# Kernel optimization log

Measured on AMD Instinct MI355X. Metric: run time of the kernel, lower is better.

The kernel has to match this reference:

```python
import jax, jax.numpy as jnp
import numpy as np

MARGIN = 0.1
NEG_INF = -1e30


def _l2norm(x):
    return x / jnp.linalg.norm(x, axis=1, keepdims=True)


def setup_inputs() -> dict:
    key = jax.random.key(0)
    ks = jax.random.split(key, 6)
    d, nNeg, Q = 128, 10, 32
    triplet_len = nNeg + 2
    n = Q * triplet_len            # 384
    m = 65536                      # XBM memory bank size
    V = 2048                       # image-id space
    P, Nn = 10, 25                 # pos / hard-neg list lengths per query
    inputs_col = _l2norm(jax.random.normal(ks[0], (n, d), dtype=jnp.float32))
    inputs_row = _l2norm(jax.random.normal(ks[1], (m, d), dtype=jnp.float32))
    targets_row = jax.random.randint(ks[2], (m,), 0, V, dtype=jnp.int64)
    qidxs = jnp.arange(Q, dtype=jnp.int64) + V  # unique query ids, disjoint from db ids
    targets_col = jax.random.randint(ks[3], (n,), 0, V, dtype=jnp.int64)
    targets_col = targets_col.at[jnp.arange(0, n, triplet_len)].set(qidxs)
    pidxs = jax.random.randint(ks[4], (Q, P), 0, V, dtype=jnp.int64)
    nnegs = jax.random.randint(ks[5], (Q, Nn), 0, V, dtype=jnp.int64)
    return {"inputs_col": inputs_col, "inputs_row": inputs_row,
            "targets_col": targets_col, "targets_row": targets_row,
            "qidxs": qidxs, "pidxs": pidxs, "nnegs": nnegs, "nNeg": nNeg}


def reference(inputs_col, inputs_row, targets_col, targets_row, qidxs, pidxs, nnegs, nNeg):
    n = inputs_col.shape[0]
    triplet_len = nNeg + 2
    query_list = jnp.arange(0, n, triplet_len)          # [Q]
    Q = query_list.shape[0]
    query_idx = targets_col[query_list]                 # [Q]

    sim_mat = inputs_col @ inputs_row.T                 # [n, m]
    sims = sim_mat[query_list]                          # [Q, m]

    # per-query lookup of pos / neg id lists (qidxs are unique)
    qidx_local = jnp.argmax(qidxs[None, :] == query_idx[:, None], axis=1)
    this_pidx = pidxs[qidx_local]                       # [Q, P]
    this_nneg = nnegs[qidx_local]                       # [Q, Nn]

    # from_batch handling (only possible when shapes match; here memory-bank case)
    if targets_col.shape[0] == targets_row.shape[0]:
        fb = jnp.all(targets_col == targets_row)
        trc = jnp.where(fb, targets_row.at[query_list].set(-1), targets_row)
    else:
        fb = None
        trc = targets_row

    # isin masks, vectorized across queries: [Q, m]
    pos_mask = jnp.any(targets_row[None, :, None] == this_pidx[:, None, :], axis=-1)
    neg_mask = ~jnp.any(trc[None, :, None] == this_nneg[:, None, :], axis=-1)
    if fb is not None:
        neg_mask = jnp.where(fb, neg_mask.at[:, query_list].set(False), neg_mask)

    # sort was only used to read the max -> masked max suffices
    pos_max = jnp.max(jnp.where(pos_mask, sims, NEG_INF), axis=1)   # [Q]
    neg_max = jnp.max(jnp.where(neg_mask, sims, NEG_INF), axis=1)   # [Q]

    pos_sel = pos_mask & (sims < neg_max[:, None] + MARGIN)
    neg_sel = neg_mask & (sims > jnp.maximum(0.4, pos_max)[:, None] - MARGIN)

    pos_cnt = jnp.sum(pos_sel, axis=1)
    neg_cnt = jnp.sum(neg_sel, axis=1)
    pos_loss = jnp.where(pos_cnt > 0,
                         jnp.sum(jnp.where(pos_sel, 1.0 - sims, 0.0), axis=1) / jnp.maximum(pos_cnt, 1),
                         0.0)
    neg_loss = jnp.where(neg_cnt > 0,
                         jnp.sum(jnp.where(neg_sel, sims, 0.0), axis=1) / jnp.maximum(neg_cnt, 1),
                         0.0)

    has_pos = jnp.any(pos_mask, axis=1)                 # whole block skipped if no positives
    loss = jnp.sum(jnp.where(has_pos, pos_loss + neg_loss, 0.0)) / Q
    return loss
```

## Files before the change

### kernel.cpp

```cpp
#include <hip/hip_runtime.h>

#define NEG_INF_F (-1e30f)
#define MARGIN_F 0.1f
#define TABN 4096
#define BR 256
#define NT 512

__device__ __forceinline__ unsigned fkey(float f) {
    unsigned b = __float_as_uint(f);
    return (b & 0x80000000u) ? ~b : (b | 0x80000000u);
}
__device__ __forceinline__ float fdec(unsigned k) {
    unsigned b = (k & 0x80000000u) ? (k ^ 0x80000000u) : ~k;
    return __uint_as_float(b);
}

__global__ __launch_bounds__(256) void setup_kernel(
    const float* __restrict__ inputs_col,
    const int* __restrict__ targets_col,
    const int* __restrict__ qidxs,
    const int* __restrict__ pidxs,
    const int* __restrict__ nnegs,
    unsigned* __restrict__ ptab,
    unsigned* __restrict__ ntab,
    float* __restrict__ qT,
    float* __restrict__ accums,
    unsigned* __restrict__ bar,
    int d, int Q, int P, int Nn, int triplet_len)
{
    __shared__ int qmap[32];
    const int tid = threadIdx.x;

    if (tid < Q) {
        int t = targets_col[tid * triplet_len];
        int l = 0;
        for (int i = Q - 1; i >= 0; --i) if (qidxs[i] == t) l = i;
        qmap[tid] = l;
    }
    for (int i = tid; i < TABN; i += 256) { ptab[i] = 0u; ntab[i] = 0u; }
    if (tid < 160) accums[tid] = 0.f;
    if (tid < 2) bar[tid] = 0u;
    __syncthreads();

    for (int i = tid; i < Q * P; i += 256) {
        int q = i / P, k = i - q * P;
        int id = pidxs[qmap[q] * P + k];
        if ((unsigned)id < TABN) atomicOr(&ptab[id], 1u << q);
    }
    for (int i = tid; i < Q * Nn; i += 256) {
        int q = i / Nn, k = i - q * Nn;
        int id = nnegs[qmap[q] * Nn + k];
        if ((unsigned)id < TABN) atomicOr(&ntab[id], 1u << q);
    }
    for (int i = tid; i < d * Q; i += 256) {
        int dd = i >> 5, q = i & 31;
        qT[i] = inputs_col[(size_t)(q * triplet_len) * d + dd];
    }
}

__device__ __forceinline__ void gsync(unsigned* cnt, unsigned nblk) {
    __syncthreads();
    if (threadIdx.x == 0) {
        __threadfence();
        atomicAdd(cnt, 1u);
        while (__hip_atomic_load(cnt, __ATOMIC_RELAXED, __HIP_MEMORY_SCOPE_AGENT) < nblk)
            __builtin_amdgcn_s_sleep(2);
        __threadfence();
    }
    __syncthreads();
}

__global__ __launch_bounds__(NT, 2) void fused_kernel(
    const float* __restrict__ qT,
    const float* __restrict__ rows,
    const int* __restrict__ targets_row,
    const unsigned* __restrict__ ptab,
    const unsigned* __restrict__ ntab,
    float* __restrict__ gmax,
    float* __restrict__ accums,
    unsigned* __restrict__ bar,
    float* __restrict__ out,
    int m, int nb)
{
    __shared__ float qv[128][32];
    __shared__ float rt[32][261];
    __shared__ unsigned pbm[BR], nbm[BR];
    __shared__ unsigned spk[32], snk[32];
    __shared__ float thr[2][32];
    __shared__ float wpart[8][32][5];
    __shared__ int islast;

    const int tid = threadIdx.x;
    const int bid = blockIdx.x;
    const int j0 = bid * BR;

    for (int i = tid; i < 128 * 32; i += NT) qv[i >> 5][i & 31] = qT[i];
    if (tid < 32) { spk[tid] = fkey(NEG_INF_F); snk[tid] = fkey(NEG_INF_F); }
    if (tid < BR) {
        int j = j0 + tid;
        unsigned pb = 0u, nbv = 0u;
        if (j < m) {
            int t = targets_row[j];
            if ((unsigned)t < TABN) { pb = ptab[t]; nbv = ~ntab[t]; }
            else                    { nbv = ~0u; }
        }
        pbm[tid] = pb; nbm[tid] = nbv;
    }

    const int qg = tid & 7;
    const int rg = tid >> 3;
    const int kk = tid & 7;
    const int jj = tid >> 3;

    float acc[4][4];
#pragma unroll
    for (int a = 0; a < 4; ++a)
#pragma unroll
        for (int b = 0; b < 4; ++b) acc[a][b] = 0.f;

    for (int kc = 0; kc < 128; kc += 32) {
        __syncthreads();
#pragma unroll
        for (int p = 0; p < 4; ++p) {
            int j = j0 + jj + 64 * p;
            int jc = (j < m) ? j : (m - 1);
            float4 v = *(const float4*)&rows[(size_t)jc * 128 + kc + 4 * kk];
            rt[4 * kk + 0][jj + 64 * p] = v.x;
            rt[4 * kk + 1][jj + 64 * p] = v.y;
            rt[4 * kk + 2][jj + 64 * p] = v.z;
            rt[4 * kk + 3][jj + 64 * p] = v.w;
        }
        __syncthreads();
#pragma unroll
        for (int k = 0; k < 32; ++k) {
            float4 qf = *(const float4*)&qv[kc + k][qg * 4];
            float4 rf = *(const float4*)&rt[k][rg * 4];
            const float* qp = (const float*)&qf;
            const float* rp = (const float*)&rf;
#pragma unroll
            for (int qi = 0; qi < 4; ++qi)
#pragma unroll
                for (int ri = 0; ri < 4; ++ri)
                    acc[qi][ri] = fmaf(qp[qi], rp[ri], acc[qi][ri]);
        }
    }

    unsigned pb[4], nbr[4];
#pragma unroll
    for (int r = 0; r < 4; ++r) { pb[r] = pbm[rg * 4 + r]; nbr[r] = nbm[rg * 4 + r]; }

#pragma unroll
    for (int qi = 0; qi < 4; ++qi) {
        const int q = qg * 4 + qi;
        float pmax = NEG_INF_F, nmax = NEG_INF_F;
#pragma unroll
        for (int r = 0; r < 4; ++r) {
            if ((pb[r] >> q) & 1u)  pmax = fmaxf(pmax, acc[qi][r]);
            if ((nbr[r] >> q) & 1u) nmax = fmaxf(nmax, acc[qi][r]);
        }
#pragma unroll
        for (int off = 32; off >= 8; off >>= 1) {
            pmax = fmaxf(pmax, __shfl_down(pmax, off));
            nmax = fmaxf(nmax, __shfl_down(nmax, off));
        }
        if ((tid & 63) < 8) {
            atomicMax(&spk[q], fkey(pmax));
            atomicMax(&snk[q], fkey(nmax));
        }
    }
    __syncthreads();
    if (tid < 64) {
        int side = tid >> 5, q = tid & 31;
        gmax[(size_t)tid * nb + bid] = fdec(side ? snk[q] : spk[q]);
    }

    gsync(&bar[0], (unsigned)nb);

    {
        int p = tid >> 3, c = tid & 7;
        float mv = NEG_INF_F;
        for (int b = c; b < nb; b += 8) mv = fmaxf(mv, gmax[(size_t)p * nb + b]);
#pragma unroll
        for (int msk = 1; msk <= 4; msk <<= 1) mv = fmaxf(mv, __shfl_xor(mv, msk));
        if (c == 0) thr[p >> 5][p & 31] = mv;
    }
    __syncthreads();

    const int wave = tid >> 6, lane = tid & 63;
#pragma unroll
    for (int qi = 0; qi < 4; ++qi) {
        const int q = qg * 4 + qi;
        const float posThr = thr[1][q] + MARGIN_F;
        const float negThr = fmaxf(0.4f, thr[0][q]) - MARGIN_F;
        float ps = 0.f, pc = 0.f, ns = 0.f, nc = 0.f, pmc = 0.f;
#pragma unroll
        for (int r = 0; r < 4; ++r) {
            float s = acc[qi][r];
            unsigned pm = (pb[r] >> q) & 1u;
            unsigned nm = (nbr[r] >> q) & 1u;
            pmc += (float)pm;
            if (pm && s < posThr) { ps += 1.f - s; pc += 1.f; }
            if (nm && s > negThr) { ns += s;       nc += 1.f; }
        }
#pragma unroll
        for (int off = 32; off >= 8; off >>= 1) {
            ps  += __shfl_down(ps, off);
            pc  += __shfl_down(pc, off);
            ns  += __shfl_down(ns, off);
            nc  += __shfl_down(nc, off);
            pmc += __shfl_down(pmc, off);
        }
        if (lane < 8) {
            wpart[wave][lane * 4 + qi][0] = ps;
            wpart[wave][lane * 4 + qi][1] = pc;
            wpart[wave][lane * 4 + qi][2] = ns;
            wpart[wave][lane * 4 + qi][3] = nc;
            wpart[wave][lane * 4 + qi][4] = pmc;
        }
    }
    __syncthreads();
    if (tid < 160) {
        float v = 0.f;
#pragma unroll
        for (int w = 0; w < 8; ++w) v += wpart[w][tid / 5][tid % 5];
        atomicAdd(&accums[tid], v);
    }

    __syncthreads();
    if (tid == 0) {
        __threadfence();
        unsigned old = atomicAdd(&bar[1], 1u);
        islast = (old == (unsigned)(nb - 1)) ? 1 : 0;
    }
    __syncthreads();
    if (islast) {
        if (tid == 0) __threadfence();
        __syncthreads();
        if (tid < 64) {
            float v = 0.f;
            if (tid < 32) {
                float psv = accums[tid * 5 + 0];
                float pcv = accums[tid * 5 + 1];
                float nsv = accums[tid * 5 + 2];
                float ncv = accums[tid * 5 + 3];
                float pmc = accums[tid * 5 + 4];
                float pl = (pcv > 0.f) ? psv / pcv : 0.f;
                float nl = (ncv > 0.f) ? nsv / ncv : 0.f;
                v = (pmc > 0.f) ? (pl + nl) : 0.f;
            }
#pragma unroll
            for (int off = 32; off; off >>= 1) v += __shfl_down(v, off);
            if (tid == 0) out[0] = v / 32.0f;
        }
    }
}

extern "C" void kernel_launch(void* const* d_in, const int* in_sizes, int n_in,
                              void* d_out, int out_size, void* d_ws, size_t ws_size,
                              hipStream_t stream)
{
    const float* inputs_col = (const float*)d_in[0];
    const float* inputs_row = (const float*)d_in[1];
    const int* targets_col  = (const int*)d_in[2];
    const int* targets_row  = (const int*)d_in[3];
    const int* qidxs        = (const int*)d_in[4];
    const int* pidxs        = (const int*)d_in[5];
    const int* nnegs        = (const int*)d_in[6];

    const int n  = in_sizes[2];
    int m        = in_sizes[3];
    const int Q  = in_sizes[4];
    const int P  = in_sizes[5] / Q;
    const int Nn = in_sizes[6] / Q;
    const int d  = in_sizes[0] / n;
    const int triplet_len = n / Q;

    int nb = (m + BR - 1) / BR;

    char* ws = (char*)d_ws;
    size_t off = 0;
    unsigned* ptab = (unsigned*)(ws + off); off += (size_t)TABN * 4;
    unsigned* ntab = (unsigned*)(ws + off); off += (size_t)TABN * 4;
    float* qT      = (float*)(ws + off);    off += (size_t)d * Q * 4;
    float* gmax    = (float*)(ws + off);    off += (size_t)64 * nb * 4;
    float* accums  = (float*)(ws + off);    off += (size_t)160 * 4;
    unsigned* bar  = (unsigned*)(ws + off); off += 2 * 4;
    float* out     = (float*)d_out;

    setup_kernel<<<1, 256, 0, stream>>>(inputs_col, targets_col, qidxs, pidxs, nnegs,
                                        ptab, ntab, qT, accums, bar,
                                        d, Q, P, Nn, triplet_len);

    fused_kernel<<<nb, NT, 0, stream>>>(qT, inputs_row, targets_row, ptab, ntab,
                                        gmax, accums, bar, out, m, nb);
}
```

Measured before the change: 138.3 us.

## Load row tiles directly into registers with software pipelining and atomic global max

Drops the shared-memory transpose staging of memory-bank rows. Each thread now loads its four rows straight from global into registers, with a multi-buffered prefetch of float4 chunks that overlaps the loads with the FMAs. Block size and rows per block are halved, which doubles the block count. The per-block max array and its gather scan after the grid barrier are replaced by atomicMax on 64 global keys. The risks are uncoalesced strided row loads, higher register pressure from the prefetch buffers, more blocks that must all be co-resident for the grid sync, and no bounds check when m is not a multiple of the new block size.

Result: slower. 165.6 us (+19.7%).

```diff
diff --git a/kernel.cpp b/kernel.cpp
--- a/kernel.cpp
+++ b/kernel.cpp
@@ -3,8 +3,8 @@
 #define NEG_INF_F (-1e30f)
 #define MARGIN_F 0.1f
 #define TABN 4096
-#define BR 256
-#define NT 512
+#define BR 128
+#define NT 256
 
 __device__ __forceinline__ unsigned fkey(float f) {
     unsigned b = __float_as_uint(f);
@@ -24,6 +24,7 @@
     unsigned* __restrict__ ptab,
     unsigned* __restrict__ ntab,
     float* __restrict__ qT,
+    unsigned* __restrict__ qkeys,
     float* __restrict__ accums,
     unsigned* __restrict__ bar,
     int d, int Q, int P, int Nn, int triplet_len)
@@ -38,6 +39,7 @@
         qmap[tid] = l;
     }
     for (int i = tid; i < TABN; i += 256) { ptab[i] = 0u; ntab[i] = 0u; }
+    if (tid < 2 * Q) qkeys[tid] = fkey(NEG_INF_F);
     if (tid < 160) accums[tid] = 0.f;
     if (tid < 2) bar[tid] = 0u;
     __syncthreads();
@@ -70,47 +72,62 @@
     __syncthreads();
 }
 
-__global__ __launch_bounds__(NT, 2) void fused_kernel(
+__global__ __launch_bounds__(NT) void fused_kernel(
     const float* __restrict__ qT,
     const float* __restrict__ rows,
     const int* __restrict__ targets_row,
     const unsigned* __restrict__ ptab,
     const unsigned* __restrict__ ntab,
-    float* __restrict__ gmax,
+    unsigned* __restrict__ qkeys,
     float* __restrict__ accums,
     unsigned* __restrict__ bar,
     float* __restrict__ out,
     int m, int nb)
 {
     __shared__ float qv[128][32];
-    __shared__ float rt[32][261];
-    __shared__ unsigned pbm[BR], nbm[BR];
     __shared__ unsigned spk[32], snk[32];
-    __shared__ float thr[2][32];
-    __shared__ float wpart[8][32][5];
+    __shared__ float sthr[2][32];
+    __shared__ float wpart[4][32][5];
     __shared__ int islast;
 
     const int tid = threadIdx.x;
     const int bid = blockIdx.x;
     const int j0 = bid * BR;
-
-    for (int i = tid; i < 128 * 32; i += NT) qv[i >> 5][i & 31] = qT[i];
+    const int qg = tid & 7, q0 = qg * 4;
+    const int rg = tid >> 3;
+    const int r0 = j0 + rg * 4;
+
+    for (int i = tid; i < 128 * 32; i += NT) ((float*)qv)[i] = qT[i];
     if (tid < 32) { spk[tid] = fkey(NEG_INF_F); snk[tid] = fkey(NEG_INF_F); }
-    if (tid < BR) {
-        int j = j0 + tid;
-        unsigned pb = 0u, nbv = 0u;
-        if (j < m) {
-            int t = targets_row[j];
-            if ((unsigned)t < TABN) { pb = ptab[t]; nbv = ~ntab[t]; }
-            else                    { nbv = ~0u; }
-        }
-        pbm[tid] = pb; nbm[tid] = nbv;
-    }
-
-    const int qg = tid & 7;
-    const int rg = tid >> 3;
-    const int kk = tid & 7;
-    const int jj = tid >> 3;
+
+    unsigned pb[4], nbr[4];
+#pragma unroll
+    for (int ri = 0; ri < 4; ++ri) {
+        int t = targets_row[r0 + ri];
+        if ((unsigned)t < TABN) { pb[ri] = ptab[t]; nbr[ri] = ~ntab[t]; }
+        else                    { pb[ri] = 0u; nbr[ri] = ~0u; }
+    }
+
+    const float* base = rows + (size_t)r0 * 128;
+    float4 b0[4], b1[4], b2[4], b3[4];
+
+#define LOADB(B, K4) { _Pragma("unroll") \
+    for (int ri = 0; ri < 4; ++ri) B[ri] = *(const float4*)(base + ri * 128 + (K4) * 4); }
+
+#define STEP(B, K4) { _Pragma("unroll") \
+    for (int dk = 0; dk < 4; ++dk) { \
+        float4 qf = *(const float4*)&qv[(K4) * 4 + dk][q0]; \
+        _Pragma("unroll") \
+        for (int qi = 0; qi < 4; ++qi) { \
+            float qq = ((const float*)&qf)[qi]; \
+            _Pragma("unroll") \
+            for (int ri = 0; ri < 4; ++ri) \
+                acc[qi][ri] = fmaf(qq, ((const float*)&B[ri])[dk], acc[qi][ri]); \
+        } } }
+
+    LOADB(b0, 0) LOADB(b1, 1) LOADB(b2, 2)
+
+    __syncthreads();
 
     float acc[4][4];
 #pragma unroll
@@ -118,40 +135,20 @@
 #pragma unroll
         for (int b = 0; b < 4; ++b) acc[a][b] = 0.f;
 
-    for (int kc = 0; kc < 128; kc += 32) {
-        __syncthreads();
-#pragma unroll
-        for (int p = 0; p < 4; ++p) {
-            int j = j0 + jj + 64 * p;
-            int jc = (j < m) ? j : (m - 1);
-            float4 v = *(const float4*)&rows[(size_t)jc * 128 + kc + 4 * kk];
-            rt[4 * kk + 0][jj + 64 * p] = v.x;
-            rt[4 * kk + 1][jj + 64 * p] = v.y;
-            rt[4 * kk + 2][jj + 64 * p] = v.z;
-            rt[4 * kk + 3][jj + 64 * p] = v.w;
-        }
-        __syncthreads();
-#pragma unroll
-        for (int k = 0; k < 32; ++k) {
-            float4 qf = *(const float4*)&qv[kc + k][qg * 4];
-            float4 rf = *(const float4*)&rt[k][rg * 4];
-            const float* qp = (const float*)&qf;
-            const float* rp = (const float*)&rf;
-#pragma unroll
-            for (int qi = 0; qi < 4; ++qi)
-#pragma unroll
-                for (int ri = 0; ri < 4; ++ri)
-                    acc[qi][ri] = fmaf(qp[qi], rp[ri], acc[qi][ri]);
-        }
-    }
-
-    unsigned pb[4], nbr[4];
-#pragma unroll
-    for (int r = 0; r < 4; ++r) { pb[r] = pbm[rg * 4 + r]; nbr[r] = nbm[rg * 4 + r]; }
+    for (int k4 = 0; k4 < 32; k4 += 4) {
+        if (k4 + 3 < 32) LOADB(b3, k4 + 3)
+        STEP(b0, k4 + 0)
+        if (k4 + 4 < 32) LOADB(b0, k4 + 4)
+        STEP(b1, k4 + 1)
+        if (k4 + 5 < 32) LOADB(b1, k4 + 5)
+        STEP(b2, k4 + 2)
+        if (k4 + 6 < 32) LOADB(b2, k4 + 6)
+        STEP(b3, k4 + 3)
+    }
 
 #pragma unroll
     for (int qi = 0; qi < 4; ++qi) {
-        const int q = qg * 4 + qi;
+        const int q = q0 + qi;
         float pmax = NEG_INF_F, nmax = NEG_INF_F;
 #pragma unroll
         for (int r = 0; r < 4; ++r) {
@@ -171,27 +168,23 @@
     __syncthreads();
     if (tid < 64) {
         int side = tid >> 5, q = tid & 31;
-        gmax[(size_t)tid * nb + bid] = fdec(side ? snk[q] : spk[q]);
+        atomicMax(&qkeys[q * 2 + side], side ? snk[q] : spk[q]);
     }
 
     gsync(&bar[0], (unsigned)nb);
 
-    {
-        int p = tid >> 3, c = tid & 7;
-        float mv = NEG_INF_F;
-        for (int b = c; b < nb; b += 8) mv = fmaxf(mv, gmax[(size_t)p * nb + b]);
-#pragma unroll
-        for (int msk = 1; msk <= 4; msk <<= 1) mv = fmaxf(mv, __shfl_xor(mv, msk));
-        if (c == 0) thr[p >> 5][p & 31] = mv;
+    if (tid < 64) {
+        int side = tid >> 5, q = tid & 31;
+        sthr[side][q] = fdec(qkeys[q * 2 + side]);
     }
     __syncthreads();
 
     const int wave = tid >> 6, lane = tid & 63;
 #pragma unroll
     for (int qi = 0; qi < 4; ++qi) {
-        const int q = qg * 4 + qi;
-        const float posThr = thr[1][q] + MARGIN_F;
-        const float negThr = fmaxf(0.4f, thr[0][q]) - MARGIN_F;
+        const int q = q0 + qi;
+        const float posThr = sthr[1][q] + MARGIN_F;
+        const float negThr = fmaxf(0.4f, sthr[0][q]) - MARGIN_F;
         float ps = 0.f, pc = 0.f, ns = 0.f, nc = 0.f, pmc = 0.f;
 #pragma unroll
         for (int r = 0; r < 4; ++r) {
@@ -222,7 +215,7 @@
     if (tid < 160) {
         float v = 0.f;
 #pragma unroll
-        for (int w = 0; w < 8; ++w) v += wpart[w][tid / 5][tid % 5];
+        for (int w = 0; w < 4; ++w) v += wpart[w][tid / 5][tid % 5];
         atomicAdd(&accums[tid], v);
     }
 
@@ -279,18 +272,18 @@
 
     char* ws = (char*)d_ws;
     size_t off = 0;
-    unsigned* ptab = (unsigned*)(ws + off); off += (size_t)TABN * 4;
-    unsigned* ntab = (unsigned*)(ws + off); off += (size_t)TABN * 4;
-    float* qT      = (float*)(ws + off);    off += (size_t)d * Q * 4;
-    float* gmax    = (float*)(ws + off);    off += (size_t)64 * nb * 4;
-    float* accums  = (float*)(ws + off);    off += (size_t)160 * 4;
-    unsigned* bar  = (unsigned*)(ws + off); off += 2 * 4;
-    float* out     = (float*)d_out;
+    unsigned* ptab  = (unsigned*)(ws + off); off += (size_t)TABN * 4;
+    unsigned* ntab  = (unsigned*)(ws + off); off += (size_t)TABN * 4;
+    float* qT       = (float*)(ws + off);    off += (size_t)d * Q * 4;
+    unsigned* qkeys = (unsigned*)(ws + off); off += (size_t)Q * 2 * 4;
+    float* accums   = (float*)(ws + off);    off += (size_t)160 * 4;
+    unsigned* bar   = (unsigned*)(ws + off); off += 2 * 4;
+    float* out      = (float*)d_out;
 
     setup_kernel<<<1, 256, 0, stream>>>(inputs_col, targets_col, qidxs, pidxs, nnegs,
-                                        ptab, ntab, qT, accums, bar,
+                                        ptab, ntab, qT, qkeys, accums, bar,
                                         d, Q, P, Nn, triplet_len);
 
     fused_kernel<<<nb, NT, 0, stream>>>(qT, inputs_row, targets_row, ptab, ntab,
-                                        gmax, accums, bar, out, m, nb);
-}
+                                        qkeys, accums, bar, out, m, nb);
+}
```

## Double-buffer row tiles, raise occupancy, flag-based grid barrier, per-block partial sums

Applied to the files above, without the earlier changes.

Replaces the four 32-wide K chunks with sixteen 8-wide chunks held in a double-buffered LDS tile. Each next chunk is prefetched into registers while the current one is multiplied, which cuts LDS usage and lets launch bounds ask for 4 blocks per CU instead of 2. The grid barrier now has the last arriving block set a release flag that the others poll, instead of every block polling the counter. Global float atomics for the loss accumulators are replaced by per-block partial writes that the last block sums serially. In exchange there are twice as many __syncthreads per K pass, a serial reduction over 256 blocks in the last block, and the higher occupancy needed for co-residency may squeeze registers.

Result: slower. 186.8 us (+35.1%).

```diff
diff --git a/kernel.cpp b/kernel.cpp
--- a/kernel.cpp
+++ b/kernel.cpp
@@ -24,7 +24,6 @@
     unsigned* __restrict__ ptab,
     unsigned* __restrict__ ntab,
     float* __restrict__ qT,
-    float* __restrict__ accums,
     unsigned* __restrict__ bar,
     int d, int Q, int P, int Nn, int triplet_len)
 {
@@ -38,8 +37,7 @@
         qmap[tid] = l;
     }
     for (int i = tid; i < TABN; i += 256) { ptab[i] = 0u; ntab[i] = 0u; }
-    if (tid < 160) accums[tid] = 0.f;
-    if (tid < 2) bar[tid] = 0u;
+    if (tid < 96) bar[tid] = 0u;
     __syncthreads();
 
     for (int i = tid; i < Q * P; i += 256) {
@@ -58,59 +56,80 @@
     }
 }
 
-__device__ __forceinline__ void gsync(unsigned* cnt, unsigned nblk) {
+__device__ __forceinline__ void gsync(unsigned* cnt, unsigned* flag, unsigned nblk) {
     __syncthreads();
     if (threadIdx.x == 0) {
         __threadfence();
-        atomicAdd(cnt, 1u);
-        while (__hip_atomic_load(cnt, __ATOMIC_RELAXED, __HIP_MEMORY_SCOPE_AGENT) < nblk)
-            __builtin_amdgcn_s_sleep(2);
+        unsigned old = atomicAdd(cnt, 1u);
+        if (old == nblk - 1u) {
+            __hip_atomic_store(flag, 1u, __ATOMIC_RELEASE, __HIP_MEMORY_SCOPE_AGENT);
+        } else {
+            while (__hip_atomic_load(flag, __ATOMIC_RELAXED, __HIP_MEMORY_SCOPE_AGENT) == 0u)
+                __builtin_amdgcn_s_sleep(8);
+        }
         __threadfence();
     }
     __syncthreads();
 }
 
-__global__ __launch_bounds__(NT, 2) void fused_kernel(
+__global__ __launch_bounds__(NT, 4) void fused_kernel(
     const float* __restrict__ qT,
     const float* __restrict__ rows,
     const int* __restrict__ targets_row,
     const unsigned* __restrict__ ptab,
     const unsigned* __restrict__ ntab,
     float* __restrict__ gmax,
-    float* __restrict__ accums,
+    float* __restrict__ psum,
     unsigned* __restrict__ bar,
     float* __restrict__ out,
     int m, int nb)
 {
     __shared__ float qv[128][32];
-    __shared__ float rt[32][261];
+    __shared__ float kt[2][8][264];
     __shared__ unsigned pbm[BR], nbm[BR];
     __shared__ unsigned spk[32], snk[32];
-    __shared__ float thr[2][32];
+    __shared__ float sthr[2][32];
     __shared__ float wpart[8][32][5];
+    __shared__ float fin[160];
     __shared__ int islast;
 
-    const int tid = threadIdx.x;
-    const int bid = blockIdx.x;
-    const int j0 = bid * BR;
-
-    for (int i = tid; i < 128 * 32; i += NT) qv[i >> 5][i & 31] = qT[i];
+    const int tid  = threadIdx.x;
+    const int bid  = blockIdx.x;
+    const int j0   = bid * BR;
+    const int lane = tid & 63;
+    const int wave = tid >> 6;
+    const int qg   = lane & 7, q0 = qg * 4;
+    const int rgl  = lane >> 3;
+    const int rloc = wave * 32 + rgl * 4;
+
+    for (int i = tid; i < 128 * 32 / 4; i += NT)
+        ((float4*)qv)[i] = ((const float4*)qT)[i];
     if (tid < 32) { spk[tid] = fkey(NEG_INF_F); snk[tid] = fkey(NEG_INF_F); }
     if (tid < BR) {
         int j = j0 + tid;
-        unsigned pb = 0u, nbv = 0u;
+        unsigned pbv = 0u, nbv = 0u;
         if (j < m) {
             int t = targets_row[j];
-            if ((unsigned)t < TABN) { pb = ptab[t]; nbv = ~ntab[t]; }
+            if ((unsigned)t < TABN) { pbv = ptab[t]; nbv = ~ntab[t]; }
             else                    { nbv = ~0u; }
         }
-        pbm[tid] = pb; nbm[tid] = nbv;
-    }
-
-    const int qg = tid & 7;
-    const int rg = tid >> 3;
-    const int kk = tid & 7;
-    const int jj = tid >> 3;
+        pbm[tid] = pbv; nbm[tid] = nbv;
+    }
+
+    const int sr  = tid >> 1;
+    const int k4  = tid & 1;
+    int jr = j0 + sr; if (jr >= m) jr = m - 1;
+    const float* gsrc = rows + (size_t)jr * 128 + k4 * 4;
+
+    {
+        float4 v = *(const float4*)(gsrc);
+        kt[0][k4 * 4 + 0][sr] = v.x;
+        kt[0][k4 * 4 + 1][sr] = v.y;
+        kt[0][k4 * 4 + 2][sr] = v.z;
+        kt[0][k4 * 4 + 3][sr] = v.w;
+    }
+    float4 vnext = *(const float4*)(gsrc + 8);
+    __syncthreads();
 
     float acc[4][4];
 #pragma unroll
@@ -118,23 +137,12 @@
 #pragma unroll
         for (int b = 0; b < 4; ++b) acc[a][b] = 0.f;
 
-    for (int kc = 0; kc < 128; kc += 32) {
-        __syncthreads();
-#pragma unroll
-        for (int p = 0; p < 4; ++p) {
-            int j = j0 + jj + 64 * p;
-            int jc = (j < m) ? j : (m - 1);
-            float4 v = *(const float4*)&rows[(size_t)jc * 128 + kc + 4 * kk];
-            rt[4 * kk + 0][jj + 64 * p] = v.x;
-            rt[4 * kk + 1][jj + 64 * p] = v.y;
-            rt[4 * kk + 2][jj + 64 * p] = v.z;
-            rt[4 * kk + 3][jj + 64 * p] = v.w;
-        }
-        __syncthreads();
-#pragma unroll
-        for (int k = 0; k < 32; ++k) {
-            float4 qf = *(const float4*)&qv[kc + k][qg * 4];
-            float4 rf = *(const float4*)&rt[k][rg * 4];
+    for (int c = 0; c < 16; ++c) {
+        const int B = c & 1;
+#pragma unroll
+        for (int s = 0; s < 8; ++s) {
+            float4 qf = *(const float4*)&qv[c * 8 + s][q0];
+            float4 rf = *(const float4*)&kt[B][s][rloc];
             const float* qp = (const float*)&qf;
             const float* rp = (const float*)&rf;
 #pragma unroll
@@ -143,15 +151,24 @@
                 for (int ri = 0; ri < 4; ++ri)
                     acc[qi][ri] = fmaf(qp[qi], rp[ri], acc[qi][ri]);
         }
+        if (c < 15) {
+            __syncthreads();
+            kt[B ^ 1][k4 * 4 + 0][sr] = vnext.x;
+            kt[B ^ 1][k4 * 4 + 1][sr] = vnext.y;
+            kt[B ^ 1][k4 * 4 + 2][sr] = vnext.z;
+            kt[B ^ 1][k4 * 4 + 3][sr] = vnext.w;
+            if (c < 14) vnext = *(const float4*)(gsrc + (c + 2) * 8);
+            __syncthreads();
+        }
     }
 
     unsigned pb[4], nbr[4];
 #pragma unroll
-    for (int r = 0; r < 4; ++r) { pb[r] = pbm[rg * 4 + r]; nbr[r] = nbm[rg * 4 + r]; }
+    for (int r = 0; r < 4; ++r) { pb[r] = pbm[rloc + r]; nbr[r] = nbm[rloc + r]; }
 
 #pragma unroll
     for (int qi = 0; qi < 4; ++qi) {
-        const int q = qg * 4 + qi;
+        const int q = q0 + qi;
         float pmax = NEG_INF_F, nmax = NEG_INF_F;
 #pragma unroll
         for (int r = 0; r < 4; ++r) {
@@ -163,7 +180,7 @@
             pmax = fmaxf(pmax, __shfl_down(pmax, off));
             nmax = fmaxf(nmax, __shfl_down(nmax, off));
         }
-        if ((tid & 63) < 8) {
+        if (lane < 8) {
             atomicMax(&spk[q], fkey(pmax));
             atomicMax(&snk[q], fkey(nmax));
         }
@@ -174,7 +191,7 @@
         gmax[(size_t)tid * nb + bid] = fdec(side ? snk[q] : spk[q]);
     }
 
-    gsync(&bar[0], (unsigned)nb);
+    gsync(&bar[0], &bar[32], (unsigned)nb);
 
     {
         int p = tid >> 3, c = tid & 7;
@@ -182,16 +199,15 @@
         for (int b = c; b < nb; b += 8) mv = fmaxf(mv, gmax[(size_t)p * nb + b]);
 #pragma unroll
         for (int msk = 1; msk <= 4; msk <<= 1) mv = fmaxf(mv, __shfl_xor(mv, msk));
-        if (c == 0) thr[p >> 5][p & 31] = mv;
-    }
-    __syncthreads();
-
-    const int wave = tid >> 6, lane = tid & 63;
+        if (c == 0) sthr[p >> 5][p & 31] = mv;
+    }
+    __syncthreads();
+
 #pragma unroll
     for (int qi = 0; qi < 4; ++qi) {
-        const int q = qg * 4 + qi;
-        const float posThr = thr[1][q] + MARGIN_F;
-        const float negThr = fmaxf(0.4f, thr[0][q]) - MARGIN_F;
+        const int q = q0 + qi;
+        const float posThr = sthr[1][q] + MARGIN_F;
+        const float negThr = fmaxf(0.4f, sthr[0][q]) - MARGIN_F;
         float ps = 0.f, pc = 0.f, ns = 0.f, nc = 0.f, pmc = 0.f;
 #pragma unroll
         for (int r = 0; r < 4; ++r) {
@@ -223,27 +239,33 @@
         float v = 0.f;
 #pragma unroll
         for (int w = 0; w < 8; ++w) v += wpart[w][tid / 5][tid % 5];
-        atomicAdd(&accums[tid], v);
+        psum[(size_t)bid * 160 + tid] = v;
     }
 
     __syncthreads();
     if (tid == 0) {
         __threadfence();
-        unsigned old = atomicAdd(&bar[1], 1u);
+        unsigned old = atomicAdd(&bar[64], 1u);
         islast = (old == (unsigned)(nb - 1)) ? 1 : 0;
     }
     __syncthreads();
     if (islast) {
         if (tid == 0) __threadfence();
+        __syncthreads();
+        if (tid < 160) {
+            float v = 0.f;
+            for (int b = 0; b < nb; ++b) v += psum[(size_t)b * 160 + tid];
+            fin[tid] = v;
+        }
         __syncthreads();
         if (tid < 64) {
             float v = 0.f;
             if (tid < 32) {
-                float psv = accums[tid * 5 + 0];
-                float pcv = accums[tid * 5 + 1];
-                float nsv = accums[tid * 5 + 2];
-                float ncv = accums[tid * 5 + 3];
-                float pmc = accums[tid * 5 + 4];
+                float psv = fin[tid * 5 + 0];
+                float pcv = fin[tid * 5 + 1];
+                float nsv = fin[tid * 5 + 2];
+                float ncv = fin[tid * 5 + 3];
+                float pmc = fin[tid * 5 + 4];
                 float pl = (pcv > 0.f) ? psv / pcv : 0.f;
                 float nl = (ncv > 0.f) ? nsv / ncv : 0.f;
                 v = (pmc > 0.f) ? (pl + nl) : 0.f;
@@ -282,15 +304,15 @@
     unsigned* ptab = (unsigned*)(ws + off); off += (size_t)TABN * 4;
     unsigned* ntab = (unsigned*)(ws + off); off += (size_t)TABN * 4;
     float* qT      = (float*)(ws + off);    off += (size_t)d * Q * 4;
+    unsigned* bar  = (unsigned*)(ws + off); off += 96 * 4;
     float* gmax    = (float*)(ws + off);    off += (size_t)64 * nb * 4;
-    float* accums  = (float*)(ws + off);    off += (size_t)160 * 4;
-    unsigned* bar  = (unsigned*)(ws + off); off += 2 * 4;
+    float* psum    = (float*)(ws + off);    off += (size_t)nb * 160 * 4;
     float* out     = (float*)d_out;
 
     setup_kernel<<<1, 256, 0, stream>>>(inputs_col, targets_col, qidxs, pidxs, nnegs,
-                                        ptab, ntab, qT, accums, bar,
+                                        ptab, ntab, qT, bar,
                                         d, Q, P, Nn, triplet_len);
 
     fused_kernel<<<nb, NT, 0, stream>>>(qT, inputs_row, targets_row, ptab, ntab,
-                                        gmax, accums, bar, out, m, nb);
-}
+                                        gmax, psum, bar, out, m, nb);
+}
```
